# Kernel optimization log

Hardware: AMD Instinct MI355X
Metric: run time of the kernel (lower is better)

## Reference

```python
import jax, jax.numpy as jnp
import numpy as np

N = 100000       # nodes
E = 1600000      # edges (avg degree 16)
F_IN, H, C = 128, 128, 47


def setup_inputs() -> dict:
    key = jax.random.key(0)
    ks = jax.random.split(key, 12)
    def lin(k, fan_in, fan_out):
        return (jax.random.normal(k, (fan_in, fan_out), dtype=jnp.float32)
                / np.float32(np.sqrt(fan_in)))
    return {
        "x": jax.random.normal(ks[0], (N, F_IN), dtype=jnp.float32),
        "src": jax.random.randint(ks[1], (E,), 0, N, dtype=jnp.int32),
        "dst": jax.random.randint(ks[2], (E,), 0, N, dtype=jnp.int32),
        "w_self0": lin(ks[3], F_IN, H),
        "w_neigh0": lin(ks[4], F_IN, H),
        "b0": jnp.zeros((H,), jnp.float32),
        "w_self1": lin(ks[5], H, H),
        "w_neigh1": lin(ks[6], H, H),
        "b1": jnp.zeros((H,), jnp.float32),
        "w_self2": lin(ks[7], H, C),
        "w_neigh2": lin(ks[8], H, C),
        "b2": jnp.zeros((C,), jnp.float32),
    }


def _sage_layer(h, src, dst, w_self, w_neigh, b):
    # mean-aggregate neighbor features: gather h[src], scatter-add to dst
    agg = jax.ops.segment_sum(h[src], dst, num_segments=N)        # [N, d]
    deg = jax.ops.segment_sum(jnp.ones((src.shape[0], 1), h.dtype), dst,
                              num_segments=N)                     # [N, 1]
    mean = agg / jnp.maximum(deg, 1.0)
    # DGL SAGEConv('mean'): fc_self(h_dst) + fc_neigh(mean) + bias
    return h @ w_self + mean @ w_neigh + b


def reference(x, src, dst,
              w_self0, w_neigh0, b0,
              w_self1, w_neigh1, b1,
              w_self2, w_neigh2, b2):
    h = _sage_layer(x, src, dst, w_self0, w_neigh0, b0)
    h = jax.nn.relu(h)  # dropout is identity in eval mode
    h = _sage_layer(h, src, dst, w_self1, w_neigh1, b1)
    h = jax.nn.relu(h)
    h = _sage_layer(h, src, dst, w_self2, w_neigh2, b2)
    return h
```

## Files before the change

kernel.cpp:

```cpp
#include <hip/hip_runtime.h>

typedef unsigned int u32;
typedef unsigned short u16;
typedef __attribute__((ext_vector_type(8))) short short8;
typedef __attribute__((ext_vector_type(4))) float f32x4;

#define POOLCAP 65536
#define IDXMASK 0x1ffff
#define BUCKCAP 12288

__device__ __forceinline__ u16 f2bf(float f) {
    u32 u = __float_as_uint(f);
    u32 r = (u + 0x7fffu + ((u >> 16) & 1u)) >> 16;
    return (u16)r;
}
__device__ __forceinline__ float bf2f(u32 lo16) { return __uint_as_float(lo16 << 16); }

__device__ __forceinline__ void acc_u4p(float2* a, uint4 v) {
    u32 w[4] = {v.x, v.y, v.z, v.w};
#pragma unroll
    for (int i = 0; i < 4; i++) {
        a[i].x += __uint_as_float(w[i] << 16);
        a[i].y += __uint_as_float(w[i] & 0xffff0000u);
    }
}

#define TILE 4096
__global__ __launch_bounds__(512) void scatter_prep(const int* __restrict__ src,
                                                    const int* __restrict__ dst,
                                                    int* __restrict__ cursor,
                                                    uint2* __restrict__ pairs, int E, int NS,
                                                    const float* __restrict__ ws0, const float* __restrict__ wn0, u16* __restrict__ wt0,
                                                    const float* __restrict__ ws1, const float* __restrict__ wn1, u16* __restrict__ wt1,
                                                    const float* __restrict__ ws2, const float* __restrict__ wn2, u16* __restrict__ wt2) {
    if (blockIdx.x >= NS) {
        int local = blockIdx.x - NS;
        const float *ws, *wn;
        u16* wt;
        int dout, HW;
        if (local < 64)       { ws = ws0; wn = wn0; wt = wt0; dout = 128; HW = 128; }
        else if (local < 128) { ws = ws1; wn = wn1; wt = wt1; dout = 128; HW = 128; local -= 64; }
        else                  { ws = ws2; wn = wn2; wt = wt2; dout = 47;  HW = 64;  local -= 128; }
        int idx = local * 512 + threadIdx.x;
        int n = idx >> 7, k = idx & 127;
        float v = 0.f;
        if (n < HW) { if (n < dout) v = ws[k * dout + n]; }
        else { int nn = n - HW; if (nn < dout) v = wn[k * dout + nn]; }
        wt[idx] = f2bf(v);
        return;
    }
    __shared__ uint2 sp[TILE];
    __shared__ int s_cnt[256], s_off[256], s_gpos[256], s_cnt2[256];
    const int tid = threadIdx.x;
    const int base = blockIdx.x * TILE;
    const int tn = min(TILE, E - base);
    if (tid < 256) { s_cnt[tid] = 0; s_cnt2[tid] = 0; }
    __syncthreads();
    int d[8], s[8];
#pragma unroll
    for (int j = 0; j < 8; j++) {
        int k = tid + j * 512;
        if (k < tn) {
            d[j] = dst[base + k];
            s[j] = src[base + k];
            atomicAdd(&s_cnt[d[j] >> 9], 1);
        } else d[j] = -1;
    }
    __syncthreads();
    if (tid < 256) s_off[tid] = s_cnt[tid];
    __syncthreads();
    for (int off = 1; off < 256; off <<= 1) {
        int v = 0;
        if (tid < 256 && tid >= off) v = s_off[tid - off];
        __syncthreads();
        if (tid < 256) s_off[tid] += v;
        __syncthreads();
    }
    if (tid < 256 && s_cnt[tid] > 0) s_gpos[tid] = atomicAdd(&cursor[tid], s_cnt[tid]);
    __syncthreads();
#pragma unroll
    for (int j = 0; j < 8; j++) {
        if (d[j] >= 0) {
            int b = d[j] >> 9;
            int p = atomicAdd(&s_cnt2[b], 1);
            sp[s_off[b] - s_cnt[b] + p] = make_uint2((u32)d[j], (u32)s[j]);
        }
    }
    __syncthreads();
    for (int k = tid; k < tn; k += 512) {
        uint2 pr = sp[k];
        int b = (int)(pr.x >> 9);
        int pos = s_gpos[b] + (k - (s_off[b] - s_cnt[b]));
        if (pos < BUCKCAP)
            pairs[(size_t)b * BUCKCAP + pos] = pr;
    }
}

__global__ __launch_bounds__(512) void build_csr3(const uint2* __restrict__ pairs,
                                                  const int* __restrict__ cursor,
                                                  float* __restrict__ invd,
                                                  int* __restrict__ colsF,
                                                  uint2* __restrict__ pool,
                                                  int* __restrict__ gcnt,
                                                  int Nn) {
    __shared__ int s_fix[512 * 32];
    __shared__ int s_cnt[512];
    const int tid = threadIdx.x;
    const int d0 = blockIdx.x * 512;
    const int nd = min(512, Nn - d0);
    const size_t base = (size_t)blockIdx.x * BUCKCAP;
    const int n = min(cursor[blockIdx.x], BUCKCAP);
    s_cnt[tid] = 0;
    __syncthreads();
    for (int k = tid; k < n; k += 512) {
        uint2 pr = pairs[base + k];
        int dl = (int)pr.x - d0;
        int p = atomicAdd(&s_cnt[dl], 1);
        if (p < 32) s_fix[dl * 32 + p] = (int)pr.y;
        else {
            int q = atomicAdd(gcnt, 1);
            if (q < POOLCAP) pool[q] = make_uint2(pr.x, pr.y);
        }
    }
    __syncthreads();
    if (tid < nd) invd[d0 + tid] = 1.0f / (float)max(s_cnt[tid], 1);
    int4* dst4 = (int4*)(colsF + (size_t)d0 * 32);
    for (int k = tid; k < 512 * 32 / 4; k += 512) {
        int node = k >> 3;
        int cnt = s_cnt[node];
        int dg = min(cnt, 0x7fff) << 17;
        int sb = (k & 7) * 4;
        int4 v;
        v.x = ((sb + 0 < cnt) ? s_fix[k * 4 + 0] : Nn) | dg;
        v.y = ((sb + 1 < cnt) ? s_fix[k * 4 + 1] : Nn) | dg;
        v.z = ((sb + 2 < cnt) ? s_fix[k * 4 + 2] : Nn) | dg;
        v.w = ((sb + 3 < cnt) ? s_fix[k * 4 + 3] : Nn) | dg;
        dst4[k] = v;
    }
}

#define KDIM 128
#define KP 136

template <int NCOLS, bool AF32>
__global__ __launch_bounds__(256) void gemm_bf16(const void* __restrict__ Ap,
                                                 const u16* __restrict__ Bt,
                                                 u16* __restrict__ C, int M) {
    __shared__ u16 As[64 * KP];
    __shared__ u16 Bs[128 * KP];
    const int row0 = blockIdx.x * 64;
    const int col0 = blockIdx.y * 128;
    const int tid = threadIdx.x;

#pragma unroll
    for (int i = 0; i < 4; i++) {
        int idx = tid + i * 256;
        int r = idx >> 4, c = idx & 15;
        uint4 v = make_uint4(0, 0, 0, 0);
        if (row0 + r < M) {
            if (AF32) {
                const float* Af = (const float*)Ap;
                const float4* rowp = (const float4*)(Af + (size_t)(row0 + r) * KDIM);
                float4 f0 = rowp[2 * c];
                float4 f1 = rowp[2 * c + 1];
                v.x = (u32)f2bf(f0.x) | ((u32)f2bf(f0.y) << 16);
                v.y = (u32)f2bf(f0.z) | ((u32)f2bf(f0.w) << 16);
                v.z = (u32)f2bf(f1.x) | ((u32)f2bf(f1.y) << 16);
                v.w = (u32)f2bf(f1.z) | ((u32)f2bf(f1.w) << 16);
            } else {
                const u16* Ab = (const u16*)Ap;
                v = ((const uint4*)(Ab + (size_t)(row0 + r) * KDIM))[c];
            }
        }
        ((uint4*)(As + r * KP))[c] = v;
    }
#pragma unroll
    for (int i = 0; i < 8; i++) {
        int idx = tid + i * 256;
        int r = idx >> 4, c = idx & 15;
        uint4 v = ((const uint4*)(Bt + (size_t)(col0 + r) * KDIM))[c];
        ((uint4*)(Bs + r * KP))[c] = v;
    }
    __syncthreads();

    const int lane = tid & 63, wave = tid >> 6;
    const int quad = lane >> 4, l16 = lane & 15;
    const int wcol = wave * 32;

    f32x4 acc[4][2];
#pragma unroll
    for (int mt = 0; mt < 4; mt++)
#pragma unroll
        for (int nt = 0; nt < 2; nt++) acc[mt][nt] = (f32x4){0.f, 0.f, 0.f, 0.f};

#pragma unroll
    for (int kc = 0; kc < 4; kc++) {
        short8 a[4], b[2];
#pragma unroll
        for (int mt = 0; mt < 4; mt++)
            a[mt] = *(const short8*)(As + (size_t)(mt * 16 + l16) * KP + kc * 32 + quad * 8);
#pragma unroll
        for (int nt = 0; nt < 2; nt++)
            b[nt] = *(const short8*)(Bs + (size_t)(wcol + nt * 16 + l16) * KP + kc * 32 + quad * 8);
#pragma unroll
        for (int mt = 0; mt < 4; mt++)
#pragma unroll
            for (int nt = 0; nt < 2; nt++)
                acc[mt][nt] = __builtin_amdgcn_mfma_f32_16x16x32_bf16(a[mt], b[nt], acc[mt][nt], 0, 0, 0);
    }

    __syncthreads();
#pragma unroll
    for (int mt = 0; mt < 4; mt++)
#pragma unroll
        for (int i = 0; i < 4; i++) {
            int rl = mt * 16 + quad * 4 + i;
#pragma unroll
            for (int nt = 0; nt < 2; nt++)
                As[rl * KP + wcol + nt * 16 + l16] = f2bf(acc[mt][nt][i]);
        }
    __syncthreads();
#pragma unroll
    for (int it = 0; it < 4; it++) {
        int idx = tid + it * 256;
        int r = idx >> 4, c8 = idx & 15;
        if (row0 + r <= M)
            *(uint4*)(C + (size_t)(row0 + r) * NCOLS + col0 + c8 * 8) =
                *(const uint4*)(As + r * KP + c8 * 8);
    }
}

template <bool RELU>
__global__ __launch_bounds__(256) void agg128f_k(const u16* __restrict__ out2,
                                                 const int* __restrict__ colsF,
                                                 const float* __restrict__ invd,
                                                 const float* __restrict__ bias,
                                                 const uint2* __restrict__ pool,
                                                 const int* __restrict__ gcnt,
                                                 u16* __restrict__ outp, int Mn) {
    int wave = threadIdx.x >> 6, lane = threadIdx.x & 63;
    int node = blockIdx.x * 4 + wave;
    if (node >= Mn) return;
    int sub = lane >> 4, l16 = lane & 15;
    const u16* tb = out2 + 128 + 8 * l16;
    const int* cp = colsF + node * 32 + sub;
    int s0 = cp[0],  s1 = cp[4],  s2 = cp[8],  s3 = cp[12];
    int s4 = cp[16], s5 = cp[20], s6 = cp[24], s7 = cp[28];
    const int deg = __builtin_amdgcn_readfirstlane(s0 >> 17);
    s0 &= IDXMASK; s1 &= IDXMASK; s2 &= IDXMASK; s3 &= IDXMASK;
    s4 &= IDXMASK; s5 &= IDXMASK; s6 &= IDXMASK; s7 &= IDXMASK;
    float id = invd[node];
    uint4 sv = *(const uint4*)(out2 + (size_t)node * 256 + 8 * l16);
    float4 b0 = *(const float4*)(bias + 8 * l16);
    float4 b1 = *(const float4*)(bias + 8 * l16 + 4);
    uint4 v0 = *(const uint4*)(tb + (size_t)s0 * 256);
    uint4 v1 = *(const uint4*)(tb + (size_t)s1 * 256);
    uint4 v2 = *(const uint4*)(tb + (size_t)s2 * 256);
    uint4 v3 = *(const uint4*)(tb + (size_t)s3 * 256);
    uint4 v4 = *(const uint4*)(tb + (size_t)s4 * 256);
    uint4 v5 = *(const uint4*)(tb + (size_t)s5 * 256);
    uint4 v6 = *(const uint4*)(tb + (size_t)s6 * 256);
    uint4 v7 = *(const uint4*)(tb + (size_t)s7 * 256);
    float2 a[4];
#pragma unroll
    for (int i = 0; i < 4; i++) a[i] = make_float2(0.f, 0.f);
    acc_u4p(a, v0);
    if (deg > 4)  acc_u4p(a, v1);
    if (deg > 8)  acc_u4p(a, v2);
    if (deg > 12) acc_u4p(a, v3);
    if (deg > 16) {
        acc_u4p(a, v4);
        if (deg > 20) acc_u4p(a, v5);
        if (deg > 24) acc_u4p(a, v6);
        if (deg > 28) acc_u4p(a, v7);
    }
    if (deg > 32) {
        int cnt = min(*gcnt, POOLCAP);
        for (int j = 0; j < cnt; j++) {
            uint2 pe = pool[j];
            if ((int)pe.x == node && sub == (j & 3))
                acc_u4p(a, *(const uint4*)(tb + (size_t)pe.y * 256));
        }
    }
    float af[8] = {a[0].x, a[0].y, a[1].x, a[1].y, a[2].x, a[2].y, a[3].x, a[3].y};
#pragma unroll
    for (int j = 0; j < 8; j++) {
        af[j] += __shfl_xor(af[j], 16); af[j] += __shfl_xor(af[j], 32);
    }
    if (sub == 0) {
        float o0 = bf2f(sv.x & 0xffffu) + af[0] * id + b0.x;
        float o1 = bf2f(sv.x >> 16)     + af[1] * id + b0.y;
        float o2 = bf2f(sv.y & 0xffffu) + af[2] * id + b0.z;
        float o3 = bf2f(sv.y >> 16)     + af[3] * id + b0.w;
        float o4 = bf2f(sv.z & 0xffffu) + af[4] * id + b1.x;
        float o5 = bf2f(sv.z >> 16)     + af[5] * id + b1.y;
        float o6 = bf2f(sv.w & 0xffffu) + af[6] * id + b1.z;
        float o7 = bf2f(sv.w >> 16)     + af[7] * id + b1.w;
        if (RELU) {
            o0 = fmaxf(o0, 0.f); o1 = fmaxf(o1, 0.f); o2 = fmaxf(o2, 0.f); o3 = fmaxf(o3, 0.f);
            o4 = fmaxf(o4, 0.f); o5 = fmaxf(o5, 0.f); o6 = fmaxf(o6, 0.f); o7 = fmaxf(o7, 0.f);
        }
        uint4 w;
        w.x = (u32)f2bf(o0) | ((u32)f2bf(o1) << 16);
        w.y = (u32)f2bf(o2) | ((u32)f2bf(o3) << 16);
        w.z = (u32)f2bf(o4) | ((u32)f2bf(o5) << 16);
        w.w = (u32)f2bf(o6) | ((u32)f2bf(o7) << 16);
        *(uint4*)(outp + (size_t)node * 128 + 8 * l16) = w;
    }
}

__global__ __launch_bounds__(256) void agg_out8f_k(const u16* __restrict__ out2,
                                                   const int* __restrict__ colsF,
                                                   const float* __restrict__ invd,
                                                   const float* __restrict__ bias,
                                                   const uint2* __restrict__ pool,
                                                   const int* __restrict__ gcnt,
                                                   float* __restrict__ outp, int Mn) {
    int wave = threadIdx.x >> 6, lane = threadIdx.x & 63;
    int node = blockIdx.x * 4 + wave;
    if (node >= Mn) return;
    int e8 = lane >> 3, l8 = lane & 7;
    const u16* tb = out2 + 64 + 8 * l8;
    const int* cp = colsF + node * 32 + e8;
    int s0 = cp[0], s1 = cp[8], s2 = cp[16], s3 = cp[24];
    const int deg = __builtin_amdgcn_readfirstlane(s0 >> 17);
    s0 &= IDXMASK; s1 &= IDXMASK; s2 &= IDXMASK; s3 &= IDXMASK;
    float id = invd[node];
    uint4 sv = *(const uint4*)(out2 + (size_t)node * 128 + 8 * l8);
    uint4 v0 = *(const uint4*)(tb + (size_t)s0 * 128);
    uint4 v1 = *(const uint4*)(tb + (size_t)s1 * 128);
    uint4 v2 = *(const uint4*)(tb + (size_t)s2 * 128);
    uint4 v3 = *(const uint4*)(tb + (size_t)s3 * 128);
    float2 a[4];
#pragma unroll
    for (int i = 0; i < 4; i++) a[i] = make_float2(0.f, 0.f);
    acc_u4p(a, v0);
    if (deg > 8)  acc_u4p(a, v1);
    if (deg > 16) acc_u4p(a, v2);
    if (deg > 24) acc_u4p(a, v3);
    if (deg > 32) {
        int cnt = min(*gcnt, POOLCAP);
        for (int j = 0; j < cnt; j++) {
            uint2 pe = pool[j];
            if ((int)pe.x == node && e8 == (j & 7))
                acc_u4p(a, *(const uint4*)(tb + (size_t)pe.y * 128));
        }
    }
    float af[8] = {a[0].x, a[0].y, a[1].x, a[1].y, a[2].x, a[2].y, a[3].x, a[3].y};
#pragma unroll
    for (int j = 0; j < 8; j++) {
        af[j] += __shfl_xor(af[j], 8); af[j] += __shfl_xor(af[j], 16); af[j] += __shfl_xor(af[j], 32);
    }
    if (e8 == 0) {
        u32 sw[4] = {sv.x, sv.y, sv.z, sv.w};
        float* orow = outp + (size_t)node * 47;
#pragma unroll
        for (int j = 0; j < 8; j++) {
            int c = 8 * l8 + j;
            if (c < 47) {
                float s = bf2f((j & 1) ? (sw[j >> 1] >> 16) : (sw[j >> 1] & 0xffffu));
                orow[c] = s + af[j] * id + bias[c];
            }
        }
    }
}


extern "C" void kernel_launch(void* const* d_in, const int* in_sizes, int n_in,
                              void* d_out, int out_size, void* d_ws, size_t ws_size,
                              hipStream_t stream) {
    const float* x   = (const float*)d_in[0];
    const int*   src = (const int*)d_in[1];
    const int*   dst = (const int*)d_in[2];
    const float* ws0 = (const float*)d_in[3];
    const float* wn0 = (const float*)d_in[4];
    const float* b0  = (const float*)d_in[5];
    const float* ws1 = (const float*)d_in[6];
    const float* wn1 = (const float*)d_in[7];
    const float* b1  = (const float*)d_in[8];
    const float* ws2 = (const float*)d_in[9];
    const float* wn2 = (const float*)d_in[10];
    const float* b2  = (const float*)d_in[11];

    const int Nn = in_sizes[0] / 128;
    const int E  = in_sizes[1];
    const int nBuckets = (Nn + 511) / 512;
    const int NnPad = nBuckets * 512;
    const int NS = (E + TILE - 1) / TILE;

    char* p = (char*)d_ws;
    auto alloc = [&](size_t bytes) -> void* {
        void* r = (void*)p;
        p += (bytes + 255) & ~(size_t)255;
        return r;
    };
    u16*   bufA   = (u16*)alloc((size_t)Nn * 128 * 2);
    u16*   out2   = (u16*)alloc(((size_t)Nn * 256 + 256) * 2);
    u16*   wt0    = (u16*)alloc(256 * 128 * 2);
    u16*   wt1    = (u16*)alloc(256 * 128 * 2);
    u16*   wt2    = (u16*)alloc(128 * 128 * 2);
    float* invd   = (float*)alloc((size_t)Nn * 4);
    int*   colsF  = (int*)alloc((size_t)NnPad * 32 * 4);
    uint2* pool   = (uint2*)alloc((size_t)POOLCAP * 8);
    int*   ctrl   = (int*)alloc(257 * 4);
    int*   cursor = ctrl;
    int*   gcnt   = ctrl + 256;
    uint2* pairs  = (uint2*)out2;

    hipMemsetAsync(ctrl, 0, 257 * 4, stream);

    scatter_prep<<<NS + 160, 512, 0, stream>>>(src, dst, cursor, pairs, E, NS,
                                               ws0, wn0, wt0, ws1, wn1, wt1, ws2, wn2, wt2);
    build_csr3<<<nBuckets, 512, 0, stream>>>(pairs, cursor, invd, colsF, pool, gcnt, Nn);

    dim3 ggrid((Nn + 63) / 64, 2);
    dim3 ggrid1((Nn + 63) / 64, 1);
    const int aggGrid = (Nn + 3) / 4;
    gemm_bf16<256, true><<<ggrid, 256, 0, stream>>>(x, wt0, out2, Nn);
    agg128f_k<true><<<aggGrid, 256, 0, stream>>>(out2, colsF, invd, b0, pool, gcnt, bufA, Nn);
    gemm_bf16<256, false><<<ggrid, 256, 0, stream>>>(bufA, wt1, out2, Nn);
    agg128f_k<true><<<aggGrid, 256, 0, stream>>>(out2, colsF, invd, b1, pool, gcnt, bufA, Nn);
    gemm_bf16<128, false><<<ggrid1, 256, 0, stream>>>(bufA, wt2, out2, Nn);
    agg_out8f_k<<<aggGrid, 256, 0, stream>>>(out2, colsF, invd, b2, pool, gcnt, (float*)d_out, Nn);
}
```

Before: 371.9 us.

## Fuse CSR build and first-layer GEMM into one heterogeneous-block launch

Merges the bucketed CSR construction kernel and the layer-0 fp32→bf16 GEMM into a single launch. The first nBuckets blocks build the CSR and the rest compute GEMM tiles. Because the two are independent, this removes a launch boundary and lets the GEMM overlap the irregular CSR build. To fit the shared LDS budget with 256 threads, the CSR build now handles each bucket in two halves of 256 nodes and reads the pairs list twice. The pairs staging buffer moves from out2 to bufA so it does not collide with the GEMM output.

```diff
diff --git a/kernel.cpp b/kernel.cpp
--- a/kernel.cpp
+++ b/kernel.cpp
@@ -96,51 +96,172 @@
     }
 }
 
-__global__ __launch_bounds__(512) void build_csr3(const uint2* __restrict__ pairs,
-                                                  const int* __restrict__ cursor,
-                                                  float* __restrict__ invd,
-                                                  int* __restrict__ colsF,
-                                                  uint2* __restrict__ pool,
-                                                  int* __restrict__ gcnt,
-                                                  int Nn) {
-    __shared__ int s_fix[512 * 32];
-    __shared__ int s_cnt[512];
-    const int tid = threadIdx.x;
-    const int d0 = blockIdx.x * 512;
-    const int nd = min(512, Nn - d0);
-    const size_t base = (size_t)blockIdx.x * BUCKCAP;
-    const int n = min(cursor[blockIdx.x], BUCKCAP);
-    s_cnt[tid] = 0;
-    __syncthreads();
-    for (int k = tid; k < n; k += 512) {
-        uint2 pr = pairs[base + k];
-        int dl = (int)pr.x - d0;
-        int p = atomicAdd(&s_cnt[dl], 1);
-        if (p < 32) s_fix[dl * 32 + p] = (int)pr.y;
-        else {
-            int q = atomicAdd(gcnt, 1);
-            if (q < POOLCAP) pool[q] = make_uint2(pr.x, pr.y);
-        }
-    }
-    __syncthreads();
-    if (tid < nd) invd[d0 + tid] = 1.0f / (float)max(s_cnt[tid], 1);
-    int4* dst4 = (int4*)(colsF + (size_t)d0 * 32);
-    for (int k = tid; k < 512 * 32 / 4; k += 512) {
-        int node = k >> 3;
-        int cnt = s_cnt[node];
-        int dg = min(cnt, 0x7fff) << 17;
-        int sb = (k & 7) * 4;
-        int4 v;
-        v.x = ((sb + 0 < cnt) ? s_fix[k * 4 + 0] : Nn) | dg;
-        v.y = ((sb + 1 < cnt) ? s_fix[k * 4 + 1] : Nn) | dg;
-        v.z = ((sb + 2 < cnt) ? s_fix[k * 4 + 2] : Nn) | dg;
-        v.w = ((sb + 3 < cnt) ? s_fix[k * 4 + 3] : Nn) | dg;
-        dst4[k] = v;
-    }
-}
-
 #define KDIM 128
 #define KP 136
+#define GEMM_LDS (64 * KP * 2 + 128 * KP * 2)
+
+__global__ __launch_bounds__(256) void build_gemm0(const uint2* __restrict__ pairs,
+                                                   const int* __restrict__ cursor,
+                                                   float* __restrict__ invd,
+                                                   int* __restrict__ colsF,
+                                                   uint2* __restrict__ pool,
+                                                   int* __restrict__ gcnt,
+                                                   const float* __restrict__ x,
+                                                   const u16* __restrict__ Bt,
+                                                   u16* __restrict__ C,
+                                                   int Nn, int nBuckets, int nRowTiles) {
+    __shared__ __align__(16) char lds[GEMM_LDS];
+    const int tid = threadIdx.x;
+
+    if (blockIdx.x < nBuckets) {
+        int* s_fix = (int*)lds;
+        int* s_cnt = (int*)(lds + 32768);
+        int* s_cn2 = (int*)(lds + 32768 + 2048);
+        const int b = blockIdx.x;
+        const int d0 = b * 512;
+        const int nd = min(512, Nn - d0);
+        const size_t base = (size_t)b * BUCKCAP;
+        const int n = min(cursor[b], BUCKCAP);
+        s_cnt[tid] = 0; s_cnt[tid + 256] = 0; s_cn2[tid] = 0;
+        __syncthreads();
+        for (int k = tid; k < n; k += 256) {
+            uint2 pr = pairs[base + k];
+            int dl = (int)pr.x - d0;
+            int p = atomicAdd(&s_cnt[dl], 1);
+            if (dl < 256) {
+                if (p < 32) s_fix[dl * 32 + p] = (int)pr.y;
+                else {
+                    int q = atomicAdd(gcnt, 1);
+                    if (q < POOLCAP) pool[q] = make_uint2(pr.x, pr.y);
+                }
+            }
+        }
+        __syncthreads();
+        for (int i = tid; i < nd; i += 256) invd[d0 + i] = 1.0f / (float)max(s_cnt[i], 1);
+        {
+            int4* dst4 = (int4*)(colsF + (size_t)d0 * 32);
+            for (int k = tid; k < 256 * 32 / 4; k += 256) {
+                int node = k >> 3;
+                int cnt = s_cnt[node];
+                int dg = min(cnt, 0x7fff) << 17;
+                int sb = (k & 7) * 4;
+                int4 v;
+                v.x = ((sb + 0 < cnt) ? s_fix[k * 4 + 0] : Nn) | dg;
+                v.y = ((sb + 1 < cnt) ? s_fix[k * 4 + 1] : Nn) | dg;
+                v.z = ((sb + 2 < cnt) ? s_fix[k * 4 + 2] : Nn) | dg;
+                v.w = ((sb + 3 < cnt) ? s_fix[k * 4 + 3] : Nn) | dg;
+                dst4[k] = v;
+            }
+        }
+        __syncthreads();
+        for (int k = tid; k < n; k += 256) {
+            uint2 pr = pairs[base + k];
+            int dl = (int)pr.x - d0;
+            if (dl >= 256) {
+                int p = atomicAdd(&s_cn2[dl - 256], 1);
+                if (p < 32) s_fix[(dl - 256) * 32 + p] = (int)pr.y;
+                else {
+                    int q = atomicAdd(gcnt, 1);
+                    if (q < POOLCAP) pool[q] = make_uint2(pr.x, pr.y);
+                }
+            }
+        }
+        __syncthreads();
+        {
+            int4* dst4 = (int4*)(colsF + (size_t)(d0 + 256) * 32);
+            for (int k = tid; k < 256 * 32 / 4; k += 256) {
+                int node = k >> 3;
+                int cnt = s_cnt[node + 256];
+                int dg = min(cnt, 0x7fff) << 17;
+                int sb = (k & 7) * 4;
+                int4 v;
+                v.x = ((sb + 0 < cnt) ? s_fix[k * 4 + 0] : Nn) | dg;
+                v.y = ((sb + 1 < cnt) ? s_fix[k * 4 + 1] : Nn) | dg;
+                v.z = ((sb + 2 < cnt) ? s_fix[k * 4 + 2] : Nn) | dg;
+                v.w = ((sb + 3 < cnt) ? s_fix[k * 4 + 3] : Nn) | dg;
+                dst4[k] = v;
+            }
+        }
+        return;
+    }
+    u16* As = (u16*)lds;
+    u16* Bs = (u16*)(lds + 64 * KP * 2);
+    const int g = blockIdx.x - nBuckets;
+    const int row0 = (g % nRowTiles) * 64;
+    const int col0 = (g / nRowTiles) * 128;
+    const int M = Nn;
+
+#pragma unroll
+    for (int i = 0; i < 4; i++) {
+        int idx = tid + i * 256;
+        int r = idx >> 4, c = idx & 15;
+        uint4 v = make_uint4(0, 0, 0, 0);
+        if (row0 + r < M) {
+            const float4* rowp = (const float4*)(x + (size_t)(row0 + r) * KDIM);
+            float4 f0 = rowp[2 * c];
+            float4 f1 = rowp[2 * c + 1];
+            v.x = (u32)f2bf(f0.x) | ((u32)f2bf(f0.y) << 16);
+            v.y = (u32)f2bf(f0.z) | ((u32)f2bf(f0.w) << 16);
+            v.z = (u32)f2bf(f1.x) | ((u32)f2bf(f1.y) << 16);
+            v.w = (u32)f2bf(f1.z) | ((u32)f2bf(f1.w) << 16);
+        }
+        ((uint4*)(As + r * KP))[c] = v;
+    }
+#pragma unroll
+    for (int i = 0; i < 8; i++) {
+        int idx = tid + i * 256;
+        int r = idx >> 4, c = idx & 15;
+        uint4 v = ((const uint4*)(Bt + (size_t)(col0 + r) * KDIM))[c];
+        ((uint4*)(Bs + r * KP))[c] = v;
+    }
+    __syncthreads();
+
+    const int lane = tid & 63, wave = tid >> 6;
+    const int quad = lane >> 4, l16 = lane & 15;
+    const int wcol = wave * 32;
+
+    f32x4 acc[4][2];
+#pragma unroll
+    for (int mt = 0; mt < 4; mt++)
+#pragma unroll
+        for (int nt = 0; nt < 2; nt++) acc[mt][nt] = (f32x4){0.f, 0.f, 0.f, 0.f};
+
+#pragma unroll
+    for (int kc = 0; kc < 4; kc++) {
+        short8 a[4], bfr[2];
+#pragma unroll
+        for (int mt = 0; mt < 4; mt++)
+            a[mt] = *(const short8*)(As + (size_t)(mt * 16 + l16) * KP + kc * 32 + quad * 8);
+#pragma unroll
+        for (int nt = 0; nt < 2; nt++)
+            bfr[nt] = *(const short8*)(Bs + (size_t)(wcol + nt * 16 + l16) * KP + kc * 32 + quad * 8);
+#pragma unroll
+        for (int mt = 0; mt < 4; mt++)
+#pragma unroll
+            for (int nt = 0; nt < 2; nt++)
+                acc[mt][nt] = __builtin_amdgcn_mfma_f32_16x16x32_bf16(a[mt], bfr[nt], acc[mt][nt], 0, 0, 0);
+    }
+
+    __syncthreads();
+#pragma unroll
+    for (int mt = 0; mt < 4; mt++)
+#pragma unroll
+        for (int i = 0; i < 4; i++) {
+            int rl = mt * 16 + quad * 4 + i;
+#pragma unroll
+            for (int nt = 0; nt < 2; nt++)
+                As[rl * KP + wcol + nt * 16 + l16] = f2bf(acc[mt][nt][i]);
+        }
+    __syncthreads();
+#pragma unroll
+    for (int it = 0; it < 4; it++) {
+        int idx = tid + it * 256;
+        int r = idx >> 4, c8 = idx & 15;
+        if (row0 + r <= M)
+            *(uint4*)(C + (size_t)(row0 + r) * 256 + col0 + c8 * 8) =
+                *(const uint4*)(As + r * KP + c8 * 8);
+    }
+}
 
 template <int NCOLS, bool AF32>
 __global__ __launch_bounds__(256) void gemm_bf16(const void* __restrict__ Ap,
@@ -386,6 +507,7 @@
     const int E  = in_sizes[1];
     const int nBuckets = (Nn + 511) / 512;
     const int NnPad = nBuckets * 512;
+    const int nRowTiles = (Nn + 63) / 64;
     const int NS = (E + TILE - 1) / TILE;
 
     char* p = (char*)d_ws;
@@ -405,18 +527,18 @@
     int*   ctrl   = (int*)alloc(257 * 4);
     int*   cursor = ctrl;
     int*   gcnt   = ctrl + 256;
-    uint2* pairs  = (uint2*)out2;
+    uint2* pairs  = (uint2*)bufA;
 
     hipMemsetAsync(ctrl, 0, 257 * 4, stream);
 
     scatter_prep<<<NS + 160, 512, 0, stream>>>(src, dst, cursor, pairs, E, NS,
                                                ws0, wn0, wt0, ws1, wn1, wt1, ws2, wn2, wt2);
-    build_csr3<<<nBuckets, 512, 0, stream>>>(pairs, cursor, invd, colsF, pool, gcnt, Nn);
-
-    dim3 ggrid((Nn + 63) / 64, 2);
-    dim3 ggrid1((Nn + 63) / 64, 1);
+    build_gemm0<<<nBuckets + nRowTiles * 2, 256, 0, stream>>>(pairs, cursor, invd, colsF, pool, gcnt,
+                                                              x, wt0, out2, Nn, nBuckets, nRowTiles);
+
+    dim3 ggrid(nRowTiles, 2);
+    dim3 ggrid1(nRowTiles, 1);
     const int aggGrid = (Nn + 3) / 4;
-    gemm_bf16<256, true><<<ggrid, 256, 0, stream>>>(x, wt0, out2, Nn);
     agg128f_k<true><<<aggGrid, 256, 0, stream>>>(out2, colsF, invd, b0, pool, gcnt, bufA, Nn);
     gemm_bf16<256, false><<<ggrid, 256, 0, stream>>>(bufA, wt1, out2, Nn);
     agg128f_k<true><<<aggGrid, 256, 0, stream>>>(out2, colsF, invd, b1, pool, gcnt, bufA, Nn);
```

Measured after the change: 374.1 us. No clear change (+0.6%).
